# Optimization experiments

Measured on AMD Instinct MI355X. Metric: run time of the kernel, lower is better.

The kernel has to match this reference:

```python
import jax, jax.numpy as jnp
import numpy as np

B, SEQ, D = 4, 4096, 64      # batch, sequence length, head dim
BS = 32                      # block_size_sparsity
V = 512                      # relative-info embedding vocabulary
R = SEQ // BS                # block rows per batch


def setup_inputs() -> dict:
    key = jax.random.key(0)
    k1, k2, k3 = jax.random.split(key, 3)
    q = jax.random.normal(k1, (B, SEQ, D), jnp.float32)
    emb = jax.random.normal(k2, (B, V, D), jnp.float32)
    # causal lower-triangular block-sparsity layout -> nonzero indices
    rb, cb = np.tril_indices(R)
    idxs_batch = jnp.asarray(np.repeat(np.arange(B), rb.size), jnp.int32)
    idxs_row = jnp.asarray(np.tile(rb, B), jnp.int32)
    P = B * rb.size  # number of nonzero sparse blocks (= 33024)
    info = jax.random.randint(k3, (P, BS, BS), 0, V, jnp.int32)
    return {"q": q, "emb": emb, "info": info,
            "idxs_batch": idxs_batch, "idxs_row": idxs_row}


def reference(q, emb, info, idxs_batch, idxs_row):
    # out[p,i,j] = <q[b_p, r_p*BS + i, :], emb[b_p, info[p,i,j], :]>
    # Compute dense per-batch scores once, then gather per sparse block.
    scores = jnp.einsum('bmd,bvd->bmv', q, emb)            # [B, SEQ, V]
    rows = idxs_row[:, None] * BS + jnp.arange(BS, dtype=jnp.int32)  # [P, BS]
    out = scores[idxs_batch[:, None, None], rows[:, :, None], info]  # [P, BS, BS]
    return out
```

## Files before the change

### kernel.cpp

```cpp
#include <hip/hip_runtime.h>

#define Bn   4
#define SEQn 4096
#define Dn   64
#define BSn  32
#define Vn   512
#define Rn   128
#define PPB  8256

#define TM   64
#define TVb  128
#define QP   68
#define EP   132

__global__ __launch_bounds__(256) void scores_kernel(
    const float* __restrict__ q, const float* __restrict__ emb,
    float* __restrict__ scores)
{
  __shared__ float sq[Dn * QP];
  __shared__ float se[Dn * EP];

  int bx   = blockIdx.x;
  int vblk = bx & 3;
  int bblk = (bx >> 2) & 3;
  int mblk = bx >> 4;
  int m0 = mblk * TM;
  int v0 = vblk * TVb;

  const float* qbase = q   + ((size_t)bblk * SEQn + m0) * Dn;
  const float* ebase = emb + ((size_t)bblk * Vn   + v0) * Dn;

  int t = threadIdx.x;
  for (int idx = t; idx < TM * Dn / 4; idx += 256) {
    int e = idx * 4;
    int m = e >> 6;
    int d = e & 63;
    float4 x = *(const float4*)(qbase + (size_t)m * Dn + d);
    sq[(d + 0) * QP + m] = x.x;
    sq[(d + 1) * QP + m] = x.y;
    sq[(d + 2) * QP + m] = x.z;
    sq[(d + 3) * QP + m] = x.w;
  }
  for (int idx = t; idx < TVb * Dn / 4; idx += 256) {
    int e = idx * 4;
    int v = e >> 6;
    int d = e & 63;
    float4 x = *(const float4*)(ebase + (size_t)v * Dn + d);
    se[(d + 0) * EP + v] = x.x;
    se[(d + 1) * EP + v] = x.y;
    se[(d + 2) * EP + v] = x.z;
    se[(d + 3) * EP + v] = x.w;
  }
  __syncthreads();

  int tx = t & 31;
  int ty = t >> 5;
  int ml = ty * 8;
  int vl = tx * 4;

  float acc[8][4];
#pragma unroll
  for (int r = 0; r < 8; ++r)
#pragma unroll
    for (int k = 0; k < 4; ++k) acc[r][k] = 0.0f;

#pragma unroll 4
  for (int d = 0; d < Dn; ++d) {
    float4 qa = *(const float4*)&sq[d * QP + ml];
    float4 qb = *(const float4*)&sq[d * QP + ml + 4];
    float4 ev = *(const float4*)&se[d * EP + vl];
    float qr[8] = {qa.x, qa.y, qa.z, qa.w, qb.x, qb.y, qb.z, qb.w};
    float ek[4] = {ev.x, ev.y, ev.z, ev.w};
#pragma unroll
    for (int r = 0; r < 8; ++r)
#pragma unroll
      for (int k = 0; k < 4; ++k) acc[r][k] += qr[r] * ek[k];
  }

  float* obase = scores + ((size_t)bblk * SEQn + m0) * Vn + v0;
#pragma unroll
  for (int r = 0; r < 8; ++r) {
    float4 st = {acc[r][0], acc[r][1], acc[r][2], acc[r][3]};
    *(float4*)(obase + (size_t)(ml + r) * Vn + vl) = st;
  }
}

#define GCHUNK 32

__global__ __launch_bounds__(512, 4) void gather_kernel(
    const float* __restrict__ scores, const int* __restrict__ info,
    float* __restrict__ out)
{
  __shared__ float slab[BSn * Vn];

  int cid = blockIdx.x;
  int b   = blockIdx.y;

  int g = 0;
  while (16 * (g + 1) * (g + 2) <= cid) ++g;
  int local = cid - 16 * g * (g + 1);
  int rq    = local / (g + 1);
  int chunk = local - rq * (g + 1);
  int r     = 32 * g + rq;
  int np    = min(GCHUNK, (r + 1) - chunk * GCHUNK);
  size_t p0 = (size_t)b * PPB + ((size_t)r * (r + 1)) / 2 + (size_t)chunk * GCHUNK;

  int tid = threadIdx.x;
  int sub = tid >> 8;
  int t   = tid & 255;
  int rowoff = (t >> 3) << 9;

  const int4* info4 = (const int4*)info;
  float4*     out4  = (float4*)out;

  int4 ivA[8];
#pragma unroll
  for (int k = 0; k < 8; ++k) {
    int pp = 2 * k + sub;
    size_t p = p0 + (pp < np ? pp : 0);
    ivA[k] = info4[p * 256 + t];
  }

  {
    const float4* src = (const float4*)(scores + ((size_t)b * SEQn + (size_t)r * BSn) * Vn);
    float4* dst = (float4*)slab;
    for (int idx = tid; idx < BSn * Vn / 4; idx += 512) dst[idx] = src[idx];
  }
  __syncthreads();

  int4 ivB[8];
  if (np > 16) {
#pragma unroll
    for (int k = 0; k < 8; ++k) {
      int pp = 16 + 2 * k + sub;
      size_t p = p0 + (pp < np ? pp : 0);
      ivB[k] = info4[p * 256 + t];
    }
  }

#pragma unroll
  for (int k = 0; k < 8; ++k) {
    int pp = 2 * k + sub;
    if (pp < np) {
      float4 o;
      o.x = slab[rowoff + ivA[k].x];
      o.y = slab[rowoff + ivA[k].y];
      o.z = slab[rowoff + ivA[k].z];
      o.w = slab[rowoff + ivA[k].w];
      out4[(p0 + pp) * 256 + t] = o;
    }
  }

  if (np > 16) {
#pragma unroll
    for (int k = 0; k < 8; ++k) {
      int pp = 16 + 2 * k + sub;
      if (pp < np) {
        float4 o;
        o.x = slab[rowoff + ivB[k].x];
        o.y = slab[rowoff + ivB[k].y];
        o.z = slab[rowoff + ivB[k].z];
        o.w = slab[rowoff + ivB[k].w];
        out4[(p0 + pp) * 256 + t] = o;
      }
    }
  }
}

extern "C" void kernel_launch(void* const* d_in, const int* in_sizes, int n_in,
                              void* d_out, int out_size, void* d_ws, size_t ws_size,
                              hipStream_t stream) {
  const float* q    = (const float*)d_in[0];
  const float* emb  = (const float*)d_in[1];
  const int*   info = (const int*)d_in[2];

  float* scores = (float*)d_ws;
  float* out    = (float*)d_out;

  int gemm_blocks = (SEQn / TM) * Bn * (Vn / TVb);
  scores_kernel<<<gemm_blocks, 256, 0, stream>>>(q, emb, scores);

  dim3 ggrid(320, Bn);
  gather_kernel<<<ggrid, 512, 0, stream>>>(scores, info, out);
}
```

Baseline: 274.0 us.

## Fuse score GEMM into gather kernel, computing per-row score slab in LDS

Replaces the two-kernel pipeline (dense scores GEMM to workspace, then gather) with one kernel that computes the 32x512 score slab for a block row directly into shared memory and gathers from it. Each workgroup handles a pair of rows (r and 127-r) to balance the triangular work, and info loads are software-pipelined in groups of four. This removes the global round-trip of the scores tensor and one launch. In exchange it uses only 256 workgroups of 1024 threads with a large LDS footprint, and it reloads emb for every row, which may limit occupancy.

```diff
diff --git a/kernel.cpp b/kernel.cpp
--- a/kernel.cpp
+++ b/kernel.cpp
@@ -8,161 +8,138 @@
 #define Rn   128
 #define PPB  8256
 
-#define TM   64
-#define TVb  128
-#define QP   68
-#define EP   132
 
-__global__ __launch_bounds__(256) void scores_kernel(
-    const float* __restrict__ q, const float* __restrict__ emb,
-    float* __restrict__ scores)
-{
-  __shared__ float sq[Dn * QP];
-  __shared__ float se[Dn * EP];
+#define SEP  258
+#define QWS  68
 
-  int bx   = blockIdx.x;
-  int vblk = bx & 3;
-  int bblk = (bx >> 2) & 3;
-  int mblk = bx >> 4;
-  int m0 = mblk * TM;
-  int v0 = vblk * TVb;
-
-  const float* qbase = q   + ((size_t)bblk * SEQn + m0) * Dn;
-  const float* ebase = emb + ((size_t)bblk * Vn   + v0) * Dn;
-
-  int t = threadIdx.x;
-  for (int idx = t; idx < TM * Dn / 4; idx += 256) {
-    int e = idx * 4;
-    int m = e >> 6;
-    int d = e & 63;
-    float4 x = *(const float4*)(qbase + (size_t)m * Dn + d);
-    sq[(d + 0) * QP + m] = x.x;
-    sq[(d + 1) * QP + m] = x.y;
-    sq[(d + 2) * QP + m] = x.z;
-    sq[(d + 3) * QP + m] = x.w;
-  }
-  for (int idx = t; idx < TVb * Dn / 4; idx += 256) {
-    int e = idx * 4;
-    int v = e >> 6;
-    int d = e & 63;
-    float4 x = *(const float4*)(ebase + (size_t)v * Dn + d);
-    se[(d + 0) * EP + v] = x.x;
-    se[(d + 1) * EP + v] = x.y;
-    se[(d + 2) * EP + v] = x.z;
-    se[(d + 3) * EP + v] = x.w;
-  }
-  __syncthreads();
-
-  int tx = t & 31;
-  int ty = t >> 5;
-  int ml = ty * 8;
-  int vl = tx * 4;
-
-  float acc[8][4];
-#pragma unroll
-  for (int r = 0; r < 8; ++r)
-#pragma unroll
-    for (int k = 0; k < 4; ++k) acc[r][k] = 0.0f;
-
-#pragma unroll 4
-  for (int d = 0; d < Dn; ++d) {
-    float4 qa = *(const float4*)&sq[d * QP + ml];
-    float4 qb = *(const float4*)&sq[d * QP + ml + 4];
-    float4 ev = *(const float4*)&se[d * EP + vl];
-    float qr[8] = {qa.x, qa.y, qa.z, qa.w, qb.x, qb.y, qb.z, qb.w};
-    float ek[4] = {ev.x, ev.y, ev.z, ev.w};
-#pragma unroll
-    for (int r = 0; r < 8; ++r)
-#pragma unroll
-      for (int k = 0; k < 4; ++k) acc[r][k] += qr[r] * ek[k];
+#define LOADI(R0, R1, R2, R3, itb)                                        \
+  {                                                                       \
+    int p0_ = ((itb) + 0) * 4 + sub, p1_ = ((itb) + 1) * 4 + sub;         \
+    int p2_ = ((itb) + 2) * 4 + sub, p3_ = ((itb) + 3) * 4 + sub;         \
+    R0 = info4[(base + (size_t)(p0_ <= r ? p0_ : 0)) * 256 + t];          \
+    R1 = info4[(base + (size_t)(p1_ <= r ? p1_ : 0)) * 256 + t];          \
+    R2 = info4[(base + (size_t)(p2_ <= r ? p2_ : 0)) * 256 + t];          \
+    R3 = info4[(base + (size_t)(p3_ <= r ? p3_ : 0)) * 256 + t];          \
   }
 
-  float* obase = scores + ((size_t)bblk * SEQn + m0) * Vn + v0;
-#pragma unroll
-  for (int r = 0; r < 8; ++r) {
-    float4 st = {acc[r][0], acc[r][1], acc[r][2], acc[r][3]};
-    *(float4*)(obase + (size_t)(ml + r) * Vn + vl) = st;
+#define PROC1(RV, pp)                                                     \
+  if ((pp) <= r) {                                                        \
+    float4 o_;                                                            \
+    o_.x = slab[rowoff + RV.x];                                           \
+    o_.y = slab[rowoff + RV.y];                                           \
+    o_.z = slab[rowoff + RV.z];                                           \
+    o_.w = slab[rowoff + RV.w];                                           \
+    out4[(base + (size_t)(pp)) * 256 + t] = o_;                           \
   }
-}
 
-#define GCHUNK 32
+#define PROCI(R0, R1, R2, R3, itb)                                        \
+  {                                                                       \
+    PROC1(R0, ((itb) + 0) * 4 + sub);                                     \
+    PROC1(R1, ((itb) + 1) * 4 + sub);                                     \
+    PROC1(R2, ((itb) + 2) * 4 + sub);                                     \
+    PROC1(R3, ((itb) + 3) * 4 + sub);                                     \
+  }
 
-__global__ __launch_bounds__(512, 4) void gather_kernel(
-    const float* __restrict__ scores, const int* __restrict__ info,
-    float* __restrict__ out)
+__global__ __launch_bounds__(1024, 4) void fused_kernel(
+    const float* __restrict__ q, const float* __restrict__ emb,
+    const int* __restrict__ info, float* __restrict__ out)
 {
+  __shared__ float sq[32 * QWS];
+  __shared__ float se[Dn * SEP];
   __shared__ float slab[BSn * Vn];
 
-  int cid = blockIdx.x;
-  int b   = blockIdx.y;
+  const int pair = blockIdx.x;
+  const int b    = blockIdx.y;
+  const int tid  = threadIdx.x;
 
-  int g = 0;
-  while (16 * (g + 1) * (g + 2) <= cid) ++g;
-  int local = cid - 16 * g * (g + 1);
-  int rq    = local / (g + 1);
-  int chunk = local - rq * (g + 1);
-  int r     = 32 * g + rq;
-  int np    = min(GCHUNK, (r + 1) - chunk * GCHUNK);
-  size_t p0 = (size_t)b * PPB + ((size_t)r * (r + 1)) / 2 + (size_t)chunk * GCHUNK;
+  const int sub    = tid >> 8;
+  const int t      = tid & 255;
+  const int rowoff = (t >> 3) << 9;
 
-  int tid = threadIdx.x;
-  int sub = tid >> 8;
-  int t   = tid & 255;
-  int rowoff = (t >> 3) << 9;
+  const int rg = tid >> 7;
+  const int v2 = tid & 127;
 
-  const int4* info4 = (const int4*)info;
-  float4*     out4  = (float4*)out;
+  const int4*   info4 = (const int4*)info;
+  float4*       out4  = (float4*)out;
+  const float2* se2   = (const float2*)se;
+  float2*       slab2 = (float2*)slab;
 
-  int4 ivA[8];
+  for (int s = 0; s < 2; ++s) {
+    const int r = s ? (127 - pair) : pair;
+    const size_t base = (size_t)b * PPB + (((size_t)r * (r + 1)) >> 1);
+    const int NIT = (r + 4) >> 2;
+
+    if (tid < 512) {
+      const float4* qs4 = (const float4*)(q + ((size_t)b * SEQn + (size_t)r * BSn) * Dn);
+      float4 x = qs4[tid];
+      ((float4*)sq)[(tid >> 4) * (QWS / 4) + (tid & 15)] = x;
+    }
+
+    int4 A0, A1, A2, A3;
+    LOADI(A0, A1, A2, A3, 0);
+
+    for (int hv = 0; hv < 2; ++hv) {
+      __syncthreads();
+      {
+        const float4* es4 = (const float4*)(emb + ((size_t)b * Vn + (size_t)hv * 256) * Dn);
 #pragma unroll
-  for (int k = 0; k < 8; ++k) {
-    int pp = 2 * k + sub;
-    size_t p = p0 + (pp < np ? pp : 0);
-    ivA[k] = info4[p * 256 + t];
-  }
+        for (int k = 0; k < 4; ++k) {
+          int idx = tid + (k << 10);
+          float4 x = es4[idx];
+          int vp = idx >> 4;
+          int d0 = (idx & 15) << 2;
+          se[(d0 + 0) * SEP + vp] = x.x;
+          se[(d0 + 1) * SEP + vp] = x.y;
+          se[(d0 + 2) * SEP + vp] = x.z;
+          se[(d0 + 3) * SEP + vp] = x.w;
+        }
+      }
+      __syncthreads();
+      float2 a0 = {0.f, 0.f}, a1 = {0.f, 0.f}, a2 = {0.f, 0.f}, a3 = {0.f, 0.f};
+      const float* qb = sq + (rg * 4) * QWS;
+#pragma unroll
+      for (int d0 = 0; d0 < Dn; d0 += 4) {
+        float4 Q0 = *(const float4*)(qb + d0);
+        float4 Q1 = *(const float4*)(qb + QWS + d0);
+        float4 Q2 = *(const float4*)(qb + 2 * QWS + d0);
+        float4 Q3 = *(const float4*)(qb + 3 * QWS + d0);
+        float2 e0 = se2[(d0 + 0) * (SEP / 2) + v2];
+        float2 e1 = se2[(d0 + 1) * (SEP / 2) + v2];
+        float2 e2 = se2[(d0 + 2) * (SEP / 2) + v2];
+        float2 e3 = se2[(d0 + 3) * (SEP / 2) + v2];
+        a0.x += Q0.x * e0.x; a0.y += Q0.x * e0.y;
+        a1.x += Q1.x * e0.x; a1.y += Q1.x * e0.y;
+        a2.x += Q2.x * e0.x; a2.y += Q2.x * e0.y;
+        a3.x += Q3.x * e0.x; a3.y += Q3.x * e0.y;
+        a0.x += Q0.y * e1.x; a0.y += Q0.y * e1.y;
+        a1.x += Q1.y * e1.x; a1.y += Q1.y * e1.y;
+        a2.x += Q2.y * e1.x; a2.y += Q2.y * e1.y;
+        a3.x += Q3.y * e1.x; a3.y += Q3.y * e1.y;
+        a0.x += Q0.z * e2.x; a0.y += Q0.z * e2.y;
+        a1.x += Q1.z * e2.x; a1.y += Q1.z * e2.y;
+        a2.x += Q2.z * e2.x; a2.y += Q2.z * e2.y;
+        a3.x += Q3.z * e2.x; a3.y += Q3.z * e2.y;
+        a0.x += Q0.w * e3.x; a0.y += Q0.w * e3.y;
+        a1.x += Q1.w * e3.x; a1.y += Q1.w * e3.y;
+        a2.x += Q2.w * e3.x; a2.y += Q2.w * e3.y;
+        a3.x += Q3.w * e3.x; a3.y += Q3.w * e3.y;
+      }
+      {
+        int sb = (rg * 4) * 256 + (hv << 7) + v2;
+        slab2[sb]       = a0;
+        slab2[sb + 256] = a1;
+        slab2[sb + 512] = a2;
+        slab2[sb + 768] = a3;
+      }
+    }
+    __syncthreads();
 
-  {
-    const float4* src = (const float4*)(scores + ((size_t)b * SEQn + (size_t)r * BSn) * Vn);
-    float4* dst = (float4*)slab;
-    for (int idx = tid; idx < BSn * Vn / 4; idx += 512) dst[idx] = src[idx];
-  }
-  __syncthreads();
-
-  int4 ivB[8];
-  if (np > 16) {
-#pragma unroll
-    for (int k = 0; k < 8; ++k) {
-      int pp = 16 + 2 * k + sub;
-      size_t p = p0 + (pp < np ? pp : 0);
-      ivB[k] = info4[p * 256 + t];
-    }
-  }
-
-#pragma unroll
-  for (int k = 0; k < 8; ++k) {
-    int pp = 2 * k + sub;
-    if (pp < np) {
-      float4 o;
-      o.x = slab[rowoff + ivA[k].x];
-      o.y = slab[rowoff + ivA[k].y];
-      o.z = slab[rowoff + ivA[k].z];
-      o.w = slab[rowoff + ivA[k].w];
-      out4[(p0 + pp) * 256 + t] = o;
-    }
-  }
-
-  if (np > 16) {
-#pragma unroll
-    for (int k = 0; k < 8; ++k) {
-      int pp = 16 + 2 * k + sub;
-      if (pp < np) {
-        float4 o;
-        o.x = slab[rowoff + ivB[k].x];
-        o.y = slab[rowoff + ivB[k].y];
-        o.z = slab[rowoff + ivB[k].z];
-        o.w = slab[rowoff + ivB[k].w];
-        out4[(p0 + pp) * 256 + t] = o;
-      }
+    for (int it0 = 0; it0 < NIT; it0 += 8) {
+      int4 B0, B1, B2, B3;
+      if (it0 + 4 < NIT) LOADI(B0, B1, B2, B3, it0 + 4);
+      PROCI(A0, A1, A2, A3, it0);
+      if (it0 + 8 < NIT) LOADI(A0, A1, A2, A3, it0 + 8);
+      if (it0 + 4 < NIT) PROCI(B0, B1, B2, B3, it0 + 4);
     }
   }
 }
@@ -173,13 +150,9 @@
   const float* q    = (const float*)d_in[0];
   const float* emb  = (const float*)d_in[1];
   const int*   info = (const int*)d_in[2];
+  float* out = (float*)d_out;
+  (void)d_ws; (void)ws_size;
 
-  float* scores = (float*)d_ws;
-  float* out    = (float*)d_out;
-
-  int gemm_blocks = (SEQn / TM) * Bn * (Vn / TVb);
-  scores_kernel<<<gemm_blocks, 256, 0, stream>>>(q, emb, scores);
-
-  dim3 ggrid(320, Bn);
-  gather_kernel<<<ggrid, 512, 0, stream>>>(scores, info, out);
+  dim3 grid(64, Bn);
+  fused_kernel<<<grid, 1024, 0, stream>>>(q, emb, info, out);
 }
```

Result: no change. 276.1 us (+0.8%).
